# Kernel tuning notes

Measured on AMD Instinct MI355X. Metric: run time of the kernel, lower is better.

The kernel has to match this reference:

```python
import jax, jax.numpy as jnp
import numpy as np

N_HEAD = 16
D_MODEL = 1024
D_K = D_MODEL // N_HEAD
LN_EPS = 1e-5


def setup_inputs() -> dict:
    key = jax.random.key(0)
    ks = jax.random.split(key, 6)
    B, T = 8, 1024
    x = jax.random.normal(ks[0], (B, T, D_MODEL), dtype=jnp.float32)
    # torch Linear weight is [out,in]; store as [in,out] for x @ W
    std_qkv = np.sqrt(2.0 / (D_MODEL + D_K)).astype(np.float32)
    W_qkv = jax.random.normal(ks[1], (D_MODEL, 3 * D_MODEL), dtype=jnp.float32) * std_qkv
    b_qkv = jnp.zeros((3 * D_MODEL,), dtype=jnp.float32)
    # xavier_normal for fc: std = sqrt(2/(fan_in+fan_out))
    std_fc = np.sqrt(2.0 / (D_MODEL + D_MODEL)).astype(np.float32)
    W_fc = jax.random.normal(ks[2], (D_MODEL, D_MODEL), dtype=jnp.float32) * std_fc
    b_fc = jnp.zeros((D_MODEL,), dtype=jnp.float32)
    ln_g = jnp.ones((D_MODEL,), dtype=jnp.float32)
    ln_b = jnp.zeros((D_MODEL,), dtype=jnp.float32)
    return {"x": x, "ln_g": ln_g, "ln_b": ln_b, "W_qkv": W_qkv, "b_qkv": b_qkv,
            "W_fc": W_fc, "b_fc": b_fc}


def _layer_norm(x, g, b):
    mu = jnp.mean(x, axis=-1, keepdims=True)
    var = jnp.mean(jnp.square(x - mu), axis=-1, keepdims=True)
    return (x - mu) * jax.lax.rsqrt(var + LN_EPS) * g + b


def reference(x, ln_g, ln_b, W_qkv, b_qkv, W_fc, b_fc):
    B, T, C = x.shape
    residual = x
    h = _layer_norm(x, ln_g, ln_b)
    qkv = h @ W_qkv + b_qkv  # [B,T,3C]
    q, k, v = jnp.split(qkv, 3, axis=-1)
    # [B,T,C] -> [B,H,T,Dk]
    def heads(t):
        return t.reshape(B, T, N_HEAD, D_K).transpose(0, 2, 1, 3)
    q, k, v = heads(q), heads(k), heads(v)
    scale = 1.0 / np.sqrt(D_K).astype(np.float32)
    attn = jax.nn.softmax(jnp.einsum('bhqd,bhkd->bhqk', q, k) * scale, axis=-1)
    out = jnp.einsum('bhqk,bhkd->bhqd', attn, v)  # [B,H,T,Dk]
    out = out.transpose(0, 2, 1, 3).reshape(B, T, C)
    out = out @ W_fc + b_fc
    out = out + residual
    return (out, attn)
```

## Files before the change

### kernel.cpp

```cpp
#include <hip/hip_runtime.h>

typedef unsigned short u16;
typedef __attribute__((ext_vector_type(4))) float floatx4;
typedef __attribute__((ext_vector_type(8))) _Float16 half8;
typedef __attribute__((ext_vector_type(8))) unsigned short ushort8v;

__device__ __forceinline__ u16 f2h(float f) {
  union { _Float16 h; u16 u; } v; v.h = (_Float16)f; return v.u;
}

__device__ __forceinline__ void async_ld16(const void* g, void* l) {
  __builtin_amdgcn_global_load_lds(
      (const __attribute__((address_space(1))) void*)g,
      (__attribute__((address_space(3))) void*)l, 16, 0, 0);
}

__global__ __launch_bounds__(256)
void wtrans_kernel(const float* __restrict__ src, u16* __restrict__ dst, int K, int N) {
  __shared__ float tile[32][33];
  int t = threadIdx.x;
  int n0 = blockIdx.x * 32, k0 = blockIdx.y * 32;
  int tx = t & 31, ty = t >> 5;
#pragma unroll
  for (int i = 0; i < 4; ++i) {
    int k = ty + i * 8;
    tile[k][tx] = src[(size_t)(k0 + k) * N + n0 + tx];
  }
  __syncthreads();
#pragma unroll
  for (int i = 0; i < 4; ++i) {
    int n = ty + i * 8;
    dst[(size_t)(n0 + n) * K + k0 + tx] = f2h(tile[tx][n]);
  }
}

__global__ __launch_bounds__(256)
void ln_kernel(const float* __restrict__ x, const float* __restrict__ g,
               const float* __restrict__ bb, u16* __restrict__ h) {
  int r = blockIdx.x, t = threadIdx.x;
  int lane = t & 63, wave = t >> 6;
  const float* xr = x + (size_t)r * 1024;
  float4 xv = *(const float4*)(xr + t * 4);
  __shared__ float red[8];
  float s = xv.x + xv.y + xv.z + xv.w;
#pragma unroll
  for (int o = 32; o; o >>= 1) s += __shfl_down(s, o, 64);
  if (lane == 0) red[wave] = s;
  __syncthreads();
  float mu = (red[0] + red[1] + red[2] + red[3]) * (1.0f / 1024.0f);
  float dx = xv.x - mu, dy = xv.y - mu, dz = xv.z - mu, dw = xv.w - mu;
  float s2 = dx * dx + dy * dy + dz * dz + dw * dw;
#pragma unroll
  for (int o = 32; o; o >>= 1) s2 += __shfl_down(s2, o, 64);
  if (lane == 0) red[4 + wave] = s2;
  __syncthreads();
  float var = (red[4] + red[5] + red[6] + red[7]) * (1.0f / 1024.0f);
  float rs = rsqrtf(var + 1e-5f);
  float4 gv = *(const float4*)(g + t * 4);
  float4 bv = *(const float4*)(bb + t * 4);
  ushort4 o4;
  o4.x = f2h(dx * rs * gv.x + bv.x);
  o4.y = f2h(dy * rs * gv.y + bv.y);
  o4.z = f2h(dz * rs * gv.z + bv.z);
  o4.w = f2h(dw * rs * gv.w + bv.w);
  *(ushort4*)(h + (size_t)r * 1024 + t * 4) = o4;
}

template <int EPI>
__global__ __launch_bounds__(256, 2)
void gemm_bt(const u16* __restrict__ A, const u16* __restrict__ BT,
             const float* __restrict__ bias, const float* __restrict__ resid,
             u16* __restrict__ outh, float* __restrict__ outf,
             int M, int N, int K) {
  __shared__ u16 As[128 * 32];
  __shared__ u16 Bs[128 * 32];
  int t = threadIdx.x, lane = t & 63, wave = t >> 6;
  int m0 = blockIdx.y * 128, n0 = blockIdx.x * 128;
  int wm = (wave >> 1) * 64, wn = (wave & 1) * 64;
  floatx4 acc[4][4];
#pragma unroll
  for (int i = 0; i < 4; ++i)
#pragma unroll
    for (int j = 0; j < 4; ++j) acc[i][j] = (floatx4){0.f, 0.f, 0.f, 0.f};
  const u16* Ag = A + (size_t)(m0 + (t >> 2)) * K + (t & 3) * 8;
  const u16* Bg = BT + (size_t)(n0 + (t >> 2)) * K + (t & 3) * 8;
  u16* Asp = As + t * 8;
  u16* Bsp = Bs + t * 8;
  int qrow = lane & 15, qk = (lane >> 4) * 8;
  for (int k0 = 0; k0 < K; k0 += 32) {
    __syncthreads();
    async_ld16(Ag + k0, Asp);
    async_ld16(Ag + k0 + (size_t)64 * K, Asp + 64 * 32);
    async_ld16(Bg + k0, Bsp);
    async_ld16(Bg + k0 + (size_t)64 * K, Bsp + 64 * 32);
    __syncthreads();
    half8 af[4], bf[4];
#pragma unroll
    for (int i = 0; i < 4; ++i)
      af[i] = *(const half8*)(As + (wm + i * 16 + qrow) * 32 + qk);
#pragma unroll
    for (int j = 0; j < 4; ++j)
      bf[j] = *(const half8*)(Bs + (wn + j * 16 + qrow) * 32 + qk);
#pragma unroll
    for (int i = 0; i < 4; ++i)
#pragma unroll
      for (int j = 0; j < 4; ++j)
        acc[i][j] = __builtin_amdgcn_mfma_f32_16x16x32_f16(af[i], bf[j], acc[i][j], 0, 0, 0);
  }
#pragma unroll
  for (int i = 0; i < 4; ++i)
#pragma unroll
    for (int j = 0; j < 4; ++j)
#pragma unroll
      for (int r = 0; r < 4; ++r) {
        int row = m0 + wm + i * 16 + (lane >> 4) * 4 + r;
        int col = n0 + wn + j * 16 + (lane & 15);
        float v = acc[i][j][r] + bias[col];
        size_t idx = (size_t)row * N + col;
        if (EPI == 0) {
          outh[idx] = f2h(v);
        } else {
          outf[idx] = v + resid[idx];
        }
      }
}

__global__ __launch_bounds__(256)
void vtrans_kernel(const u16* __restrict__ qkv, u16* __restrict__ vT) {
  __shared__ u16 tile[64][80];
  int t = threadIdx.x;
  int bh = blockIdx.x >> 4, chunk = blockIdx.x & 15;
  int b = bh >> 4, h = bh & 15;
#pragma unroll
  for (int it = 0; it < 2; ++it) {
    int row = it * 32 + (t >> 3), seg = t & 7;
    const u16* src = qkv + (size_t)(b * 1024 + chunk * 64 + row) * 3072 + 2048 + h * 64 + seg * 8;
    *(ushort8v*)&tile[row][seg * 8] = *(const ushort8v*)src;
  }
  __syncthreads();
#pragma unroll
  for (int it = 0; it < 2; ++it) {
    int d = it * 32 + (t >> 3), tks = t & 7;
    ushort8v v;
#pragma unroll
    for (int e = 0; e < 8; ++e) v[e] = tile[tks * 8 + e][d];
    *(ushort8v*)(vT + ((size_t)bh * 64 + d) * 1024 + chunk * 64 + tks * 8) = v;
  }
}

__global__ __launch_bounds__(256, 2)
void attn_kernel(const u16* __restrict__ qkv, const u16* __restrict__ vT,
                 float* __restrict__ attnO, u16* __restrict__ P) {
  const int SW = 1032;
  __shared__ float s_lds[16 * SW];
  __shared__ float inv16[16];
  int t = threadIdx.x, lane = t & 63, wave = t >> 6;
  int qt = blockIdx.x & 63, bh = blockIdx.x >> 6;
  int b = bh >> 4, h = bh & 15;
  int tq0 = qt * 16;
  int m = lane & 15, qe = lane >> 4;

  const u16* qbase = qkv + (size_t)(b * 1024 + tq0 + m) * 3072 + h * 64 + qe * 8;
  half8 a0 = *(const half8*)(qbase);
  half8 a1 = *(const half8*)(qbase + 32);
#pragma unroll 4
  for (int ct = 0; ct < 16; ++ct) {
    int kt = wave * 256 + ct * 16;
    const u16* kbase = qkv + (size_t)(b * 1024 + kt + m) * 3072 + 1024 + h * 64 + qe * 8;
    half8 b0 = *(const half8*)(kbase);
    half8 b1 = *(const half8*)(kbase + 32);
    floatx4 acc = (floatx4){0.f, 0.f, 0.f, 0.f};
    acc = __builtin_amdgcn_mfma_f32_16x16x32_f16(a0, b0, acc, 0, 0, 0);
    acc = __builtin_amdgcn_mfma_f32_16x16x32_f16(a1, b1, acc, 0, 0, 0);
#pragma unroll
    for (int r = 0; r < 4; ++r)
      s_lds[(qe * 4 + r) * SW + kt + m] = acc[r] * 0.125f;
  }
  __syncthreads();

  int row = t >> 4, sub = t & 15;
  float* srow = s_lds + row * SW;
  float mx = -1e30f;
#pragma unroll 8
  for (int i = 0; i < 64; ++i) mx = fmaxf(mx, srow[sub + 16 * i]);
#pragma unroll
  for (int o = 8; o; o >>= 1) mx = fmaxf(mx, __shfl_xor(mx, o, 16));
  float sum = 0.f;
#pragma unroll 8
  for (int i = 0; i < 64; ++i) {
    float e = __expf(srow[sub + 16 * i] - mx);
    srow[sub + 16 * i] = e;
    sum += e;
  }
#pragma unroll
  for (int o = 8; o; o >>= 1) sum += __shfl_xor(sum, o, 16);
  if (sub == 0) inv16[row] = 1.0f / sum;
  __syncthreads();

  float inv = inv16[row];
  float* arow = attnO + ((size_t)(bh * 1024 + tq0 + row)) * 1024;
#pragma unroll 4
  for (int i = 0; i < 32; ++i) {
    int col = 2 * sub + 32 * i;
    float2 v = make_float2(srow[col] * inv, srow[col + 1] * inv);
    *(float2*)(arow + col) = v;
  }

  floatx4 oacc = (floatx4){0.f, 0.f, 0.f, 0.f};
  const u16* vbase = vT + ((size_t)bh * 64 + wave * 16 + m) * 1024 + qe * 8;
  const float* prow = s_lds + m * SW + qe * 8;
#pragma unroll 4
  for (int k0 = 0; k0 < 1024; k0 += 32) {
    float4 p0 = *(const float4*)(prow + k0);
    float4 p1 = *(const float4*)(prow + k0 + 4);
    half8 af;
    af[0] = (_Float16)p0.x; af[1] = (_Float16)p0.y;
    af[2] = (_Float16)p0.z; af[3] = (_Float16)p0.w;
    af[4] = (_Float16)p1.x; af[5] = (_Float16)p1.y;
    af[6] = (_Float16)p1.z; af[7] = (_Float16)p1.w;
    half8 bv = *(const half8*)(vbase + k0);
    oacc = __builtin_amdgcn_mfma_f32_16x16x32_f16(af, bv, oacc, 0, 0, 0);
  }
#pragma unroll
  for (int r = 0; r < 4; ++r) {
    int orow = qe * 4 + r;
    float v = oacc[r] * inv16[orow];
    P[(size_t)(b * 1024 + tq0 + orow) * 1024 + h * 64 + wave * 16 + m] = f2h(v);
  }
}

extern "C" void kernel_launch(void* const* d_in, const int* in_sizes, int n_in,
                              void* d_out, int out_size, void* d_ws, size_t ws_size,
                              hipStream_t stream) {
  const float* x     = (const float*)d_in[0];
  const float* ln_g  = (const float*)d_in[1];
  const float* ln_b  = (const float*)d_in[2];
  const float* W_qkv = (const float*)d_in[3];
  const float* b_qkv = (const float*)d_in[4];
  const float* W_fc  = (const float*)d_in[5];
  const float* b_fc  = (const float*)d_in[6];
  float* outp  = (float*)d_out;
  float* attnp = outp + (size_t)8 * 1024 * 1024;

  u16* ws    = (u16*)d_ws;
  u16* h     = ws;
  u16* wqkvT = ws + 8388608;
  u16* wfcT  = ws + 11534336;
  u16* qkv   = ws + 12582912;
  u16* vT    = ws + 37748736;
  u16* P     = h;

  wtrans_kernel<<<dim3(96, 32), 256, 0, stream>>>(W_qkv, wqkvT, 1024, 3072);
  wtrans_kernel<<<dim3(32, 32), 256, 0, stream>>>(W_fc, wfcT, 1024, 1024);
  ln_kernel<<<8192, 256, 0, stream>>>(x, ln_g, ln_b, h);
  gemm_bt<0><<<dim3(24, 64), 256, 0, stream>>>(h, wqkvT, b_qkv, nullptr, qkv, nullptr,
                                               8192, 3072, 1024);
  vtrans_kernel<<<2048, 256, 0, stream>>>(qkv, vT);
  attn_kernel<<<8192, 256, 0, stream>>>(qkv, vT, attnp, P);
  gemm_bt<1><<<dim3(8, 64), 256, 0, stream>>>(P, wfcT, b_fc, x, nullptr, outp,
                                              8192, 1024, 1024);
}
```

Before: 1.022 ms.

## Keep attention scores in registers and stage fp16 probabilities in LDS

The QK^T results now stay in registers as 16 accumulator tiles per wave, and the row max and sum are reduced with shuffles plus a small cross-wave LDS exchange, replacing the fp32 score buffer in LDS. Only fp16 exponentials are written to LDS for the PV matmul, which halves LDS use and drops the fp32-to-fp16 conversion in the inner loop. Launch bounds move to 4 blocks per CU to take advantage of the smaller LDS footprint. The attention-probability output is now written with strided scalar stores (16-float runs per row) instead of float2 row-contiguous stores, and the higher register demand could limit occupancy.

```diff
diff --git a/kernel.cpp b/kernel.cpp
--- a/kernel.cpp
+++ b/kernel.cpp
@@ -148,11 +148,13 @@
   }
 }
 
-__global__ __launch_bounds__(256, 2)
+__global__ __launch_bounds__(256, 4)
 void attn_kernel(const u16* __restrict__ qkv, const u16* __restrict__ vT,
                  float* __restrict__ attnO, u16* __restrict__ P) {
-  const int SW = 1032;
-  __shared__ float s_lds[16 * SW];
+  const int SP = 1032;
+  __shared__ u16 P_lds[16 * SP];
+  __shared__ float redA[64];
+  __shared__ float redB[64];
   __shared__ float inv16[16];
   int t = threadIdx.x, lane = t & 63, wave = t >> 6;
   int qt = blockIdx.x & 63, bh = blockIdx.x >> 6;
@@ -163,68 +165,95 @@
   const u16* qbase = qkv + (size_t)(b * 1024 + tq0 + m) * 3072 + h * 64 + qe * 8;
   half8 a0 = *(const half8*)(qbase);
   half8 a1 = *(const half8*)(qbase + 32);
-#pragma unroll 4
+  floatx4 acc[16];
+#pragma unroll
   for (int ct = 0; ct < 16; ++ct) {
     int kt = wave * 256 + ct * 16;
     const u16* kbase = qkv + (size_t)(b * 1024 + kt + m) * 3072 + 1024 + h * 64 + qe * 8;
     half8 b0 = *(const half8*)(kbase);
     half8 b1 = *(const half8*)(kbase + 32);
-    floatx4 acc = (floatx4){0.f, 0.f, 0.f, 0.f};
-    acc = __builtin_amdgcn_mfma_f32_16x16x32_f16(a0, b0, acc, 0, 0, 0);
-    acc = __builtin_amdgcn_mfma_f32_16x16x32_f16(a1, b1, acc, 0, 0, 0);
-#pragma unroll
-    for (int r = 0; r < 4; ++r)
-      s_lds[(qe * 4 + r) * SW + kt + m] = acc[r] * 0.125f;
-  }
-  __syncthreads();
-
-  int row = t >> 4, sub = t & 15;
-  float* srow = s_lds + row * SW;
-  float mx = -1e30f;
-#pragma unroll 8
-  for (int i = 0; i < 64; ++i) mx = fmaxf(mx, srow[sub + 16 * i]);
-#pragma unroll
-  for (int o = 8; o; o >>= 1) mx = fmaxf(mx, __shfl_xor(mx, o, 16));
-  float sum = 0.f;
-#pragma unroll 8
-  for (int i = 0; i < 64; ++i) {
-    float e = __expf(srow[sub + 16 * i] - mx);
-    srow[sub + 16 * i] = e;
-    sum += e;
-  }
-#pragma unroll
-  for (int o = 8; o; o >>= 1) sum += __shfl_xor(sum, o, 16);
-  if (sub == 0) inv16[row] = 1.0f / sum;
-  __syncthreads();
-
-  float inv = inv16[row];
-  float* arow = attnO + ((size_t)(bh * 1024 + tq0 + row)) * 1024;
-#pragma unroll 4
-  for (int i = 0; i < 32; ++i) {
-    int col = 2 * sub + 32 * i;
-    float2 v = make_float2(srow[col] * inv, srow[col + 1] * inv);
-    *(float2*)(arow + col) = v;
+    floatx4 a = (floatx4){0.f, 0.f, 0.f, 0.f};
+    a = __builtin_amdgcn_mfma_f32_16x16x32_f16(a0, b0, a, 0, 0, 0);
+    a = __builtin_amdgcn_mfma_f32_16x16x32_f16(a1, b1, a, 0, 0, 0);
+#pragma unroll
+    for (int r = 0; r < 4; ++r) a[r] *= 0.125f;
+    acc[ct] = a;
+  }
+
+  float mx[4];
+#pragma unroll
+  for (int r = 0; r < 4; ++r) mx[r] = -1e30f;
+#pragma unroll
+  for (int ct = 0; ct < 16; ++ct)
+#pragma unroll
+    for (int r = 0; r < 4; ++r) mx[r] = fmaxf(mx[r], acc[ct][r]);
+#pragma unroll
+  for (int o = 8; o; o >>= 1)
+#pragma unroll
+    for (int r = 0; r < 4; ++r) mx[r] = fmaxf(mx[r], __shfl_xor(mx[r], o, 16));
+  if (m == 0) {
+#pragma unroll
+    for (int r = 0; r < 4; ++r) redA[wave * 16 + qe * 4 + r] = mx[r];
+  }
+  __syncthreads();
+  float gmax[4];
+#pragma unroll
+  for (int r = 0; r < 4; ++r) {
+    float v0 = redA[qe * 4 + r], v1 = redA[16 + qe * 4 + r];
+    float v2 = redA[32 + qe * 4 + r], v3 = redA[48 + qe * 4 + r];
+    gmax[r] = fmaxf(fmaxf(v0, v1), fmaxf(v2, v3));
+  }
+
+  float sm[4] = {0.f, 0.f, 0.f, 0.f};
+#pragma unroll
+  for (int ct = 0; ct < 16; ++ct) {
+#pragma unroll
+    for (int r = 0; r < 4; ++r) {
+      float e = __expf(acc[ct][r] - gmax[r]);
+      acc[ct][r] = e;
+      sm[r] += e;
+      P_lds[(qe * 4 + r) * SP + wave * 256 + ct * 16 + m] = f2h(e);
+    }
+  }
+#pragma unroll
+  for (int o = 8; o; o >>= 1)
+#pragma unroll
+    for (int r = 0; r < 4; ++r) sm[r] += __shfl_xor(sm[r], o, 16);
+  if (m == 0) {
+#pragma unroll
+    for (int r = 0; r < 4; ++r) redB[wave * 16 + qe * 4 + r] = sm[r];
+  }
+  __syncthreads();
+  if (t < 16) {
+    float s = redB[t] + redB[16 + t] + redB[32 + t] + redB[48 + t];
+    inv16[t] = 1.0f / s;
+  }
+  __syncthreads();
+
+  float invr[4];
+#pragma unroll
+  for (int r = 0; r < 4; ++r) invr[r] = inv16[qe * 4 + r];
+  float* abase = attnO + ((size_t)(bh * 1024 + tq0 + qe * 4)) * 1024 + wave * 256 + m;
+#pragma unroll
+  for (int r = 0; r < 4; ++r) {
+    float* arow = abase + (size_t)r * 1024;
+#pragma unroll
+    for (int ct = 0; ct < 16; ++ct) arow[ct * 16] = acc[ct][r] * invr[r];
   }
 
   floatx4 oacc = (floatx4){0.f, 0.f, 0.f, 0.f};
   const u16* vbase = vT + ((size_t)bh * 64 + wave * 16 + m) * 1024 + qe * 8;
-  const float* prow = s_lds + m * SW + qe * 8;
-#pragma unroll 4
+  const u16* prow = P_lds + m * SP + qe * 8;
+#pragma unroll 8
   for (int k0 = 0; k0 < 1024; k0 += 32) {
-    float4 p0 = *(const float4*)(prow + k0);
-    float4 p1 = *(const float4*)(prow + k0 + 4);
-    half8 af;
-    af[0] = (_Float16)p0.x; af[1] = (_Float16)p0.y;
-    af[2] = (_Float16)p0.z; af[3] = (_Float16)p0.w;
-    af[4] = (_Float16)p1.x; af[5] = (_Float16)p1.y;
-    af[6] = (_Float16)p1.z; af[7] = (_Float16)p1.w;
+    half8 af = *(const half8*)(prow + k0);
     half8 bv = *(const half8*)(vbase + k0);
     oacc = __builtin_amdgcn_mfma_f32_16x16x32_f16(af, bv, oacc, 0, 0, 0);
   }
 #pragma unroll
   for (int r = 0; r < 4; ++r) {
     int orow = qe * 4 + r;
-    float v = oacc[r] * inv16[orow];
+    float v = oacc[r] * invr[r];
     P[(size_t)(b * 1024 + tq0 + orow) * 1024 + h * 64 + wave * 16 + m] = f2h(v);
   }
 }
```

Measured after the change: 911.7 us. -10.8%, faster.
